# Optimization experiments

Measured on AMD Instinct MI355X. Metric: run time of the kernel, lower is better.

## Reference

```python
import jax, jax.numpy as jnp
import numpy as np

NEG_SLOPE = 0.2


def _gat_layer(x, src, dst, W, att_src, att_dst, bias, concat):
    # x: [N, Fin], W: [Fin, H*C], att_*: [H, C], bias: [H*C] or [C]
    N = x.shape[0]
    H, C = att_src.shape
    h = (x @ W).reshape(N, H, C)                      # node features per head
    a_src = jnp.sum(h * att_src, axis=-1)             # [N, H]
    a_dst = jnp.sum(h * att_dst, axis=-1)             # [N, H]
    e = jax.nn.leaky_relu(a_src[src] + a_dst[dst], NEG_SLOPE)  # [E, H]
    # segment softmax over destination nodes
    m = jax.ops.segment_max(e, dst, num_segments=N)   # [N, H]
    m = jnp.where(jnp.isfinite(m), m, 0.0)
    ex = jnp.exp(e - m[dst])
    s = jax.ops.segment_sum(ex, dst, num_segments=N)  # [N, H]
    alpha = ex / (s[dst] + 1e-16)                     # [E, H]
    msg = h[src] * alpha[:, :, None]                  # [E, H, C]
    out = jax.ops.segment_sum(msg, dst, num_segments=N)  # [N, H, C]
    out = out.reshape(N, H * C) if concat else out.mean(axis=1)
    return out + bias


def setup_inputs() -> dict:
    key = jax.random.key(0)
    ks = jax.random.split(key, 20)
    N, E, Fin, Cg, H = 50000, 800000, 128, 64, 4
    HC = H * Cg
    s = 0.1
    x = jax.random.normal(ks[0], (N, Fin), jnp.float32)
    edge_index = jax.random.randint(ks[1], (2, E), 0, N, dtype=jnp.int32)
    inp = {
        'x': x,
        'edge_index': edge_index,
        'W0': jax.random.normal(ks[2], (Fin, HC), jnp.float32) * s,
        'as0': jax.random.normal(ks[3], (H, Cg), jnp.float32) * s,
        'ad0': jax.random.normal(ks[4], (H, Cg), jnp.float32) * s,
        'b0': jnp.zeros((HC,), jnp.float32),
        'W1': jax.random.normal(ks[5], (HC, HC), jnp.float32) * s,
        'as1': jax.random.normal(ks[6], (H, Cg), jnp.float32) * s,
        'ad1': jax.random.normal(ks[7], (H, Cg), jnp.float32) * s,
        'b1': jnp.zeros((HC,), jnp.float32),
        'W2': jax.random.normal(ks[8], (HC, HC), jnp.float32) * s,
        'as2': jax.random.normal(ks[9], (H, Cg), jnp.float32) * s,
        'ad2': jax.random.normal(ks[10], (H, Cg), jnp.float32) * s,
        'b2': jnp.zeros((Cg,), jnp.float32),
        # linear head: 64 -> 128 -> 10
        'lw0': jax.random.normal(ks[11], (Cg, 128), jnp.float32) * s,
        'lb0': jnp.zeros((128,), jnp.float32),
        'lw1': jax.random.normal(ks[12], (128, 10), jnp.float32) * s,
        'lb1': jnp.zeros((10,), jnp.float32),
    }
    return inp


def reference(x, edge_index, W0, as0, ad0, b0, W1, as1, ad1, b1,
              W2, as2, ad2, b2, lw0, lb0, lw1, lb1):
    N = x.shape[0]
    # PyG GATConv add_self_loops=True: append self-loop edges
    loop = jnp.arange(N, dtype=edge_index.dtype)
    src = jnp.concatenate([edge_index[0], loop])
    dst = jnp.concatenate([edge_index[1], loop])
    h = _gat_layer(x, src, dst, W0, as0, ad0, b0, True)
    h = _gat_layer(h, src, dst, W1, as1, ad1, b1, True)
    h = _gat_layer(h, src, dst, W2, as2, ad2, b2, False)
    h = jax.nn.relu(h @ lw0 + lb0)
    return h @ lw1 + lb1
```

## Files before the change

kernel.cpp:

```cpp
#include <hip/hip_runtime.h>
#include <hip/hip_bf16.h>

#define HEADS 4
#define CH 64
#define HC 256

typedef __attribute__((ext_vector_type(8))) short short8;
typedef __attribute__((ext_vector_type(4))) float f32x4;
typedef __attribute__((ext_vector_type(8))) _Float16 half8;

__device__ inline unsigned short f2bf(float f){
  unsigned u = __float_as_uint(f);
  return (unsigned short)((u + 0x7FFF + ((u >> 16) & 1)) >> 16);
}


__global__ void hist_kernel(const int* __restrict__ dst, int E, int ET, int* __restrict__ cnt){
  int e = blockIdx.x * blockDim.x + threadIdx.x;
  if (e >= ET) return;
  int d = (e < E) ? dst[e] : (e - E);
  atomicAdd(&cnt[d], 1);
}

__global__ void blocksum_kernel(const int* __restrict__ cnt, int N, int* __restrict__ bsum){
  int tid = threadIdx.x;
  int i = blockIdx.x * 256 + tid;
  int v = (i < N) ? cnt[i] : 0;
  #pragma unroll
  for (int off = 32; off >= 1; off >>= 1) v += __shfl_xor(v, off);
  __shared__ int ws[4];
  if ((tid & 63) == 0) ws[tid >> 6] = v;
  __syncthreads();
  if (tid == 0) bsum[blockIdx.x] = ws[0] + ws[1] + ws[2] + ws[3];
}

__global__ void scanb_kernel(int* __restrict__ bsum, int nb){
  __shared__ int buf[256];
  int tid = threadIdx.x;
  int v = (tid < nb) ? bsum[tid] : 0;
  buf[tid] = v;
  __syncthreads();
  #pragma unroll
  for (int off = 1; off < 256; off <<= 1){
    int t = (tid >= off) ? buf[tid - off] : 0;
    __syncthreads();
    buf[tid] += t;
    __syncthreads();
  }
  if (tid < nb) bsum[tid] = buf[tid] - v;
}

__global__ void scanfinal_kernel(const int* __restrict__ cnt, const int* __restrict__ bsum,
                                 int* __restrict__ ptr, int* __restrict__ cur, int N){
  __shared__ int buf[256];
  int tid = threadIdx.x;
  int i = blockIdx.x * 256 + tid;
  int v = (i < N) ? cnt[i] : 0;
  buf[tid] = v;
  __syncthreads();
  #pragma unroll
  for (int off = 1; off < 256; off <<= 1){
    int t = (tid >= off) ? buf[tid - off] : 0;
    __syncthreads();
    buf[tid] += t;
    __syncthreads();
  }
  int exc = buf[tid] - v + bsum[blockIdx.x];
  if (i < N){
    ptr[i] = exc; cur[i] = exc;
    if (i == N - 1) ptr[N] = exc + v;
  }
}

__global__ void scatter_kernel(const int* __restrict__ src, const int* __restrict__ dst,
                               int E, int ET, int* __restrict__ cur, int* __restrict__ csr_src){
  int e = blockIdx.x * blockDim.x + threadIdx.x;
  if (e >= ET) return;
  int s, d;
  if (e < E){ s = src[e]; d = dst[e]; } else { s = e - E; d = e - E; }
  int pos = atomicAdd(&cur[d], 1);
  csr_src[pos] = s;
}


__global__ void wsplit_kernel(const float* __restrict__ W0, unsigned short* __restrict__ h0,
                              unsigned short* __restrict__ l0,
                              const float* __restrict__ W1, unsigned short* __restrict__ h1,
                              unsigned short* __restrict__ l1,
                              const float* __restrict__ W2, unsigned short* __restrict__ h2,
                              unsigned short* __restrict__ l2){
  int idx = blockIdx.x * 256 + threadIdx.x;
  const float* W; unsigned short *hi, *lo; int K;
  if (idx < 128 * HC){ W = W0; hi = h0; lo = l0; K = 128; }
  else if (idx < (128 + 256) * HC){ idx -= 128 * HC; W = W1; hi = h1; lo = l1; K = 256; }
  else { idx -= (128 + 256) * HC; W = W2; hi = h2; lo = l2; K = 256; }
  int k = idx >> 8, n = idx & 255;
  float w = W[idx];
  unsigned short hb = f2bf(w);
  float hf = __uint_as_float((unsigned)hb << 16);
  unsigned short lb = f2bf(w - hf);
  hi[(size_t)n * K + k] = hb;
  lo[(size_t)n * K + k] = lb;
}


__global__ void lwsplit_kernel(const float* __restrict__ lw0,
                               unsigned short* __restrict__ l0hi, unsigned short* __restrict__ l0lo,
                               const float* __restrict__ lw1, _Float16* __restrict__ l1T){
  int idx = blockIdx.x * 256 + threadIdx.x;
  if (idx < 8192){
    int n = idx & 127, k = idx >> 7;
    float w = lw0[k * 128 + n];
    unsigned short hb = f2bf(w);
    float hf = __uint_as_float((unsigned)hb << 16);
    unsigned short lb = f2bf(w - hf);
    l0hi[n * 64 + k] = hb;
    l0lo[n * 64 + k] = lb;
  } else if (idx < 8192 + 2048){
    int id = idx - 8192;
    int n = id & 15, k = id >> 4;
    float w = (n < 10) ? lw1[k * 10 + n] : 0.f;
    l1T[n * 128 + k] = (_Float16)w;
  }
}


__launch_bounds__(256, 2)
__global__ void gemm_mfma_kernel(const float* __restrict__ A,
                                 const unsigned short* __restrict__ BhiT,
                                 const unsigned short* __restrict__ BloT,
                                 _Float16* __restrict__ Cm,
                                 const float* __restrict__ att_s, const float* __restrict__ att_d,
                                 float* __restrict__ a_src, float* __restrict__ a_dst,
                                 int M, int K){
  __shared__ unsigned short As_hi[128][40];
  __shared__ unsigned short As_lo[128][40];
  __shared__ unsigned short Bs_hi[128][40];
  __shared__ unsigned short Bs_lo[128][40];

  int tid = threadIdx.x;
  int m0 = blockIdx.x * 128, n0 = blockIdx.y * 128;
  int wave = tid >> 6, lane = tid & 63;
  int wm = (wave >> 1) * 64, wn = (wave & 1) * 64;
  int col = lane & 15, quad = lane >> 4;

  f32x4 acc[4][4];
  #pragma unroll
  for (int a = 0; a < 4; a++)
    #pragma unroll
    for (int b = 0; b < 4; b++)
      acc[a][b] = (f32x4){0.f, 0.f, 0.f, 0.f};

  for (int k0 = 0; k0 < K; k0 += 32){
    #pragma unroll
    for (int r = 0; r < 2; r++){
      int id = r * 256 + tid;
      int m = id >> 2, q = id & 3;
      int gm = m0 + m;
      float va[8];
      if (gm < M){
        float4 v0 = *(const float4*)&A[(size_t)gm * K + k0 + q * 8];
        float4 v1 = *(const float4*)&A[(size_t)gm * K + k0 + q * 8 + 4];
        va[0]=v0.x; va[1]=v0.y; va[2]=v0.z; va[3]=v0.w;
        va[4]=v1.x; va[5]=v1.y; va[6]=v1.z; va[7]=v1.w;
      } else {
        #pragma unroll
        for (int j = 0; j < 8; j++) va[j] = 0.f;
      }
      short8 hi8, lo8;
      #pragma unroll
      for (int j = 0; j < 8; j++){
        unsigned short hb = f2bf(va[j]);
        float hf = __uint_as_float((unsigned)hb << 16);
        hi8[j] = (short)hb;
        lo8[j] = (short)f2bf(va[j] - hf);
      }
      *(short8*)&As_hi[m][q * 8] = hi8;
      *(short8*)&As_lo[m][q * 8] = lo8;
    }
    #pragma unroll
    for (int r = 0; r < 2; r++){
      int id = r * 256 + tid;
      int n = id >> 2, q = id & 3;
      size_t g = (size_t)(n0 + n) * K + k0 + q * 8;
      *(short8*)&Bs_hi[n][q * 8] = *(const short8*)&BhiT[g];
      *(short8*)&Bs_lo[n][q * 8] = *(const short8*)&BloT[g];
    }
    __syncthreads();

    short8 af[4][2], bf[4][2];
    #pragma unroll
    for (int t = 0; t < 4; t++){
      af[t][0] = *(const short8*)&As_hi[wm + t * 16 + col][quad * 8];
      af[t][1] = *(const short8*)&As_lo[wm + t * 16 + col][quad * 8];
      bf[t][0] = *(const short8*)&Bs_hi[wn + t * 16 + col][quad * 8];
      bf[t][1] = *(const short8*)&Bs_lo[wn + t * 16 + col][quad * 8];
    }
    #pragma unroll
    for (int mt = 0; mt < 4; mt++)
      #pragma unroll
      for (int nt = 0; nt < 4; nt++){
        acc[mt][nt] = __builtin_amdgcn_mfma_f32_16x16x32_bf16(af[mt][0], bf[nt][0], acc[mt][nt], 0, 0, 0);
        acc[mt][nt] = __builtin_amdgcn_mfma_f32_16x16x32_bf16(af[mt][1], bf[nt][0], acc[mt][nt], 0, 0, 0);
        acc[mt][nt] = __builtin_amdgcn_mfma_f32_16x16x32_bf16(af[mt][0], bf[nt][1], acc[mt][nt], 0, 0, 0);
      }
    __syncthreads();
  }

  #pragma unroll
  for (int mt = 0; mt < 4; mt++)
    #pragma unroll
    for (int nt = 0; nt < 4; nt++){
      int colg = n0 + wn + nt * 16 + col;
      #pragma unroll
      for (int r = 0; r < 4; r++){
        int row = m0 + wm + mt * 16 + quad * 4 + r;
        if (row < M) Cm[(size_t)row * HC + colg] = (_Float16)acc[mt][nt][r];
      }
    }

  int head = (n0 + wn) >> 6;
  float asv[4], adv[4];
  #pragma unroll
  for (int nt = 0; nt < 4; nt++){
    asv[nt] = att_s[head * CH + nt * 16 + col];
    adv[nt] = att_d[head * CH + nt * 16 + col];
  }
  #pragma unroll
  for (int mt = 0; mt < 4; mt++){
    float sp[4] = {0.f,0.f,0.f,0.f}, dp[4] = {0.f,0.f,0.f,0.f};
    #pragma unroll
    for (int nt = 0; nt < 4; nt++)
      #pragma unroll
      for (int r = 0; r < 4; r++){
        sp[r] += acc[mt][nt][r] * asv[nt];
        dp[r] += acc[mt][nt][r] * adv[nt];
      }
    #pragma unroll
    for (int off = 1; off <= 8; off <<= 1)
      #pragma unroll
      for (int r = 0; r < 4; r++){
        sp[r] += __shfl_xor(sp[r], off);
        dp[r] += __shfl_xor(dp[r], off);
      }
    if (col == 0){
      #pragma unroll
      for (int r = 0; r < 4; r++){
        int row = m0 + wm + mt * 16 + quad * 4 + r;
        if (row < M){
          a_src[row * HEADS + head] = sp[r];
          a_dst[row * HEADS + head] = dp[r];
        }
      }
    }
  }
}


__global__ void agg_kernel(const _Float16* __restrict__ h, const float* __restrict__ a_src,
                           const float* __restrict__ a_dst, const int* __restrict__ ptr,
                           const int* __restrict__ csr_src, const float* __restrict__ bias,
                           float* __restrict__ out, int N, int mean_mode,
                           const float* __restrict__ b2){
  __shared__ float sm[HEADS][CH];
  int n = blockIdx.x;
  int head = threadIdx.x >> 6;
  int lane = threadIdx.x & 63;
  int eg = lane >> 3, c8 = lane & 7;
  int beg = ptr[n], end = ptr[n + 1];
  float adst = a_dst[n * HEADS + head];

  float acc[8] = {0.f,0.f,0.f,0.f,0.f,0.f,0.f,0.f};
  float ss = 0.f;
  for (int i = beg + eg; i < end; i += 8){
    int s = csr_src[i];
    float e = a_src[s * HEADS + head] + adst;
    e = e > 0.f ? e : 0.2f * e;
    float w = __expf(e);
    half8 hv = *(const half8*)&h[(size_t)s * HC + head * CH + c8 * 8];
    #pragma unroll
    for (int j = 0; j < 8; j++) acc[j] += w * (float)hv[j];
    ss += w;
  }
  #pragma unroll
  for (int off = 8; off <= 32; off <<= 1){
    #pragma unroll
    for (int j = 0; j < 8; j++) acc[j] += __shfl_xor(acc[j], off);
    ss += __shfl_xor(ss, off);
  }
  float inv = 1.f / (ss + 1e-16f);
  #pragma unroll
  for (int j = 0; j < 8; j++) acc[j] *= inv;

  if (!mean_mode){
    if (eg == 0){
      float* op = &out[(size_t)n * HC + head * CH + c8 * 8];
      const float* bp = &bias[head * CH + c8 * 8];
      #pragma unroll
      for (int j = 0; j < 8; j++) op[j] = acc[j] + bp[j];
    }
  } else {
    if (eg == 0){
      #pragma unroll
      for (int j = 0; j < 8; j++) sm[head][c8 * 8 + j] = acc[j];
    }
    __syncthreads();
    int t = threadIdx.x;
    if (t < CH)
      out[(size_t)n * CH + t] =
        0.25f * (sm[0][t] + sm[1][t] + sm[2][t] + sm[3][t]) + b2[t];
  }
}


__launch_bounds__(256, 2)
__global__ void head_mfma_kernel(const float* __restrict__ f2,
                                 const unsigned short* __restrict__ lw0hiT,
                                 const unsigned short* __restrict__ lw0loT,
                                 const _Float16* __restrict__ lw1T,
                                 const float* __restrict__ lb0,
                                 const float* __restrict__ lb1,
                                 float* __restrict__ outp, int N){
  __shared__ __align__(16) unsigned short L[27648];
  __shared__ __align__(16) _Float16 Ls[16][136];
  const int tid = threadIdx.x;
  const int wave = tid >> 6, lane = tid & 63;
  const int col = lane & 15, quad = lane >> 4;
  const int m0 = blockIdx.x * 64;

  { int n = tid >> 4, k = (tid & 15) * 8;
    *(half8*)&Ls[n][k] = *(const half8*)&lw1T[n * 128 + k]; }

  #pragma unroll
  for (int r = 0; r < 2; r++){
    int id = r * 256 + tid;
    int m = id >> 3, q = id & 7;
    int gm = m0 + m;
    float va[8];
    if (gm < N){
      float4 v0 = *(const float4*)&f2[(size_t)gm * CH + q * 8];
      float4 v1 = *(const float4*)&f2[(size_t)gm * CH + q * 8 + 4];
      va[0]=v0.x; va[1]=v0.y; va[2]=v0.z; va[3]=v0.w;
      va[4]=v1.x; va[5]=v1.y; va[6]=v1.z; va[7]=v1.w;
    } else {
      #pragma unroll
      for (int j = 0; j < 8; j++) va[j] = 0.f;
    }
    short8 hi8, lo8;
    #pragma unroll
    for (int j = 0; j < 8; j++){
      unsigned short hb = f2bf(va[j]);
      float hf = __uint_as_float((unsigned)hb << 16);
      hi8[j] = (short)hb;
      lo8[j] = (short)f2bf(va[j] - hf);
    }
    *(short8*)&L[m * 72 + q * 8] = hi8;
    *(short8*)&L[4608 + m * 72 + q * 8] = lo8;
  }
  #pragma unroll
  for (int r = 0; r < 4; r++){
    int id = r * 256 + tid;
    int n = id >> 3, q = id & 7;
    *(short8*)&L[9216 + n * 72 + q * 8]  = *(const short8*)&lw0hiT[n * 64 + q * 8];
    *(short8*)&L[18432 + n * 72 + q * 8] = *(const short8*)&lw0loT[n * 64 + q * 8];
  }
  __syncthreads();

  const int wn = wave * 32;
  f32x4 acc[4][2];
  #pragma unroll
  for (int a = 0; a < 4; a++)
    #pragma unroll
    for (int b = 0; b < 2; b++) acc[a][b] = (f32x4){0.f,0.f,0.f,0.f};

  #pragma unroll
  for (int ks = 0; ks < 2; ks++){
    int k = ks * 32 + quad * 8;
    short8 ah[4], al[4], bh[2], bl[2];
    #pragma unroll
    for (int mt = 0; mt < 4; mt++){
      ah[mt] = *(short8*)&L[(mt * 16 + col) * 72 + k];
      al[mt] = *(short8*)&L[4608 + (mt * 16 + col) * 72 + k];
    }
    #pragma unroll
    for (int nt = 0; nt < 2; nt++){
      bh[nt] = *(short8*)&L[9216 + (wn + nt * 16 + col) * 72 + k];
      bl[nt] = *(short8*)&L[18432 + (wn + nt * 16 + col) * 72 + k];
    }
    #pragma unroll
    for (int mt = 0; mt < 4; mt++)
      #pragma unroll
      for (int nt = 0; nt < 2; nt++){
        acc[mt][nt] = __builtin_amdgcn_mfma_f32_16x16x32_bf16(ah[mt], bh[nt], acc[mt][nt], 0, 0, 0);
        acc[mt][nt] = __builtin_amdgcn_mfma_f32_16x16x32_bf16(al[mt], bh[nt], acc[mt][nt], 0, 0, 0);
        acc[mt][nt] = __builtin_amdgcn_mfma_f32_16x16x32_bf16(ah[mt], bl[nt], acc[mt][nt], 0, 0, 0);
      }
  }
  __syncthreads();

  _Float16* Zp = (_Float16*)L;
  #pragma unroll
  for (int nt = 0; nt < 2; nt++){
    int n = wn + nt * 16 + col;
    float b = lb0[n];
    #pragma unroll
    for (int mt = 0; mt < 4; mt++)
      #pragma unroll
      for (int r2 = 0; r2 < 4; r2++){
        int m = mt * 16 + quad * 4 + r2;
        float z = acc[mt][nt][r2] + b;
        Zp[m * 136 + n] = (_Float16)fmaxf(z, 0.f);
      }
  }
  __syncthreads();

  f32x4 acc2 = (f32x4){0.f,0.f,0.f,0.f};
  #pragma unroll
  for (int ks = 0; ks < 4; ks++){
    int k = ks * 32 + quad * 8;
    half8 a2 = *(half8*)&Zp[(wave * 16 + col) * 136 + k];
    half8 b2v = *(half8*)&Ls[col][k];
    acc2 = __builtin_amdgcn_mfma_f32_16x16x32_f16(a2, b2v, acc2, 0, 0, 0);
  }
  if (col < 10){
    float bb = lb1[col];
    #pragma unroll
    for (int r2 = 0; r2 < 4; r2++){
      int row = m0 + wave * 16 + quad * 4 + r2;
      if (row < N) outp[(size_t)row * 10 + col] = acc2[r2] + bb;
    }
  }
}


extern "C" void kernel_launch(void* const* d_in, const int* in_sizes, int n_in,
                              void* d_out, int out_size, void* d_ws, size_t ws_size,
                              hipStream_t stream) {
  const float* x   = (const float*)d_in[0];
  const int*   ei  = (const int*)d_in[1];
  const float* W0  = (const float*)d_in[2];
  const float* as0 = (const float*)d_in[3];
  const float* ad0 = (const float*)d_in[4];
  const float* b0  = (const float*)d_in[5];
  const float* W1  = (const float*)d_in[6];
  const float* as1 = (const float*)d_in[7];
  const float* ad1 = (const float*)d_in[8];
  const float* b1  = (const float*)d_in[9];
  const float* W2  = (const float*)d_in[10];
  const float* as2 = (const float*)d_in[11];
  const float* ad2 = (const float*)d_in[12];
  const float* b2  = (const float*)d_in[13];
  const float* lw0 = (const float*)d_in[14];
  const float* lb0 = (const float*)d_in[15];
  const float* lw1 = (const float*)d_in[16];
  const float* lb1 = (const float*)d_in[17];
  float* outp = (float*)d_out;

  int N  = in_sizes[0] / 128;
  int E  = in_sizes[1] / 2;
  int ET = E + N;
  int nb = (N + 255) / 256;

  char* ws = (char*)d_ws;
  float* F       = (float*)ws;    ws += (size_t)N * HC * sizeof(float);
  _Float16* Hb   = (_Float16*)ws; ws += (size_t)N * HC * sizeof(_Float16);
  float* a_s = (float*)ws; ws += (size_t)N * HEADS * sizeof(float);
  float* a_d = (float*)ws; ws += (size_t)N * HEADS * sizeof(float);
  int* cnt   = (int*)ws;   ws += (size_t)N * sizeof(int);
  int* cur   = (int*)ws;   ws += (size_t)N * sizeof(int);
  int* ptrA  = (int*)ws;   ws += (size_t)(N + 1) * sizeof(int);
  int* bsum  = (int*)ws;   ws += (size_t)nb * sizeof(int);
  int* csr   = (int*)ws;   ws += (size_t)ET * sizeof(int);
  unsigned short* w0hi = (unsigned short*)ws; ws += (size_t)128 * HC * 2;
  unsigned short* w0lo = (unsigned short*)ws; ws += (size_t)128 * HC * 2;
  unsigned short* w1hi = (unsigned short*)ws; ws += (size_t)HC * HC * 2;
  unsigned short* w1lo = (unsigned short*)ws; ws += (size_t)HC * HC * 2;
  unsigned short* w2hi = (unsigned short*)ws; ws += (size_t)HC * HC * 2;
  unsigned short* w2lo = (unsigned short*)ws; ws += (size_t)HC * HC * 2;
  unsigned short* l0hi = (unsigned short*)ws; ws += (size_t)8192 * 2;
  unsigned short* l0lo = (unsigned short*)ws; ws += (size_t)8192 * 2;
  _Float16* l1T        = (_Float16*)ws;       ws += (size_t)2048 * 2;
  float* f2  = F;

  const int* srcArr = ei;
  const int* dstArr = ei + E;

  hipMemsetAsync(cnt, 0, (size_t)N * sizeof(int), stream);
  hist_kernel<<<(ET + 255) / 256, 256, 0, stream>>>(dstArr, E, ET, cnt);
  blocksum_kernel<<<nb, 256, 0, stream>>>(cnt, N, bsum);
  scanb_kernel<<<1, 256, 0, stream>>>(bsum, nb);
  scanfinal_kernel<<<nb, 256, 0, stream>>>(cnt, bsum, ptrA, cur, N);
  scatter_kernel<<<(ET + 255) / 256, 256, 0, stream>>>(srcArr, dstArr, E, ET, cur, csr);

  wsplit_kernel<<<((128 + 256 + 256) * HC) / 256, 256, 0, stream>>>(
      W0, w0hi, w0lo, W1, w1hi, w1lo, W2, w2hi, w2lo);
  lwsplit_kernel<<<(8192 + 2048 + 255) / 256, 256, 0, stream>>>(lw0, l0hi, l0lo, lw1, l1T);

  dim3 ggrid((N + 127) / 128, 2);

  gemm_mfma_kernel<<<ggrid, 256, 0, stream>>>(x, w0hi, w0lo, Hb, as0, ad0, a_s, a_d, N, 128);
  agg_kernel<<<N, 256, 0, stream>>>(Hb, a_s, a_d, ptrA, csr, b0, F, N, 0, nullptr);

  gemm_mfma_kernel<<<ggrid, 256, 0, stream>>>(F, w1hi, w1lo, Hb, as1, ad1, a_s, a_d, N, HC);
  agg_kernel<<<N, 256, 0, stream>>>(Hb, a_s, a_d, ptrA, csr, b1, F, N, 0, nullptr);

  gemm_mfma_kernel<<<ggrid, 256, 0, stream>>>(F, w2hi, w2lo, Hb, as2, ad2, a_s, a_d, N, HC);
  agg_kernel<<<N, 256, 0, stream>>>(Hb, a_s, a_d, ptrA, csr, nullptr, f2, N, 1, b2);

  head_mfma_kernel<<<(N + 63) / 64, 256, 0, stream>>>(f2, l0hi, l0lo, l1T, lb0, lb1, outp, N);
}
```

Before: 595.8 us.

## Pre-split GEMM inputs into bf16 hi/lo in producers and unroll aggregation loop

The bf16 hi/lo split of the GEMM A operand moves out of the GEMM load path. The aggregation kernel now writes hi/lo bf16 pairs directly, and a new xsplit kernel pre-splits x for the first layer. The GEMM then loads short8 halves straight into shared memory, so each of the two column blocks no longer repeats the conversion arithmetic. Separately, the aggregation edge loop is unrolled by two with independent accumulators to expose more memory-level parallelism. The cost is an extra pass over x for the split kernel, plus a separate f2 buffer for the last layer's output.

```diff
diff --git a/kernel.cpp b/kernel.cpp
--- a/kernel.cpp
+++ b/kernel.cpp
@@ -104,6 +104,25 @@
 }
 
 
+__global__ void xsplit_kernel(const float* __restrict__ x, int total4,
+                              unsigned short* __restrict__ xhi, unsigned short* __restrict__ xlo){
+  int i4 = blockIdx.x * 256 + threadIdx.x;
+  if (i4 >= total4) return;
+  float4 v = *(const float4*)&x[(size_t)i4 * 4];
+  float va[4] = {v.x, v.y, v.z, v.w};
+  unsigned short h4[4], l4[4];
+  #pragma unroll
+  for (int j = 0; j < 4; j++){
+    unsigned short hb = f2bf(va[j]);
+    float hf = __uint_as_float((unsigned)hb << 16);
+    h4[j] = hb;
+    l4[j] = f2bf(va[j] - hf);
+  }
+  *(ushort4*)&xhi[(size_t)i4 * 4] = make_ushort4(h4[0], h4[1], h4[2], h4[3]);
+  *(ushort4*)&xlo[(size_t)i4 * 4] = make_ushort4(l4[0], l4[1], l4[2], l4[3]);
+}
+
+
 __global__ void lwsplit_kernel(const float* __restrict__ lw0,
                                unsigned short* __restrict__ l0hi, unsigned short* __restrict__ l0lo,
                                const float* __restrict__ lw1, _Float16* __restrict__ l1T){
@@ -126,7 +145,8 @@
 
 
 __launch_bounds__(256, 2)
-__global__ void gemm_mfma_kernel(const float* __restrict__ A,
+__global__ void gemm_mfma_kernel(const unsigned short* __restrict__ Ahi,
+                                 const unsigned short* __restrict__ Alo,
                                  const unsigned short* __restrict__ BhiT,
                                  const unsigned short* __restrict__ BloT,
                                  _Float16* __restrict__ Cm,
@@ -151,32 +171,22 @@
     for (int b = 0; b < 4; b++)
       acc[a][b] = (f32x4){0.f, 0.f, 0.f, 0.f};
 
+  const short8 zero8 = (short8){0,0,0,0,0,0,0,0};
+
   for (int k0 = 0; k0 < K; k0 += 32){
     #pragma unroll
     for (int r = 0; r < 2; r++){
       int id = r * 256 + tid;
       int m = id >> 2, q = id & 3;
       int gm = m0 + m;
-      float va[8];
+      size_t g = (size_t)gm * K + k0 + q * 8;
+      short8 vh = zero8, vl = zero8;
       if (gm < M){
-        float4 v0 = *(const float4*)&A[(size_t)gm * K + k0 + q * 8];
-        float4 v1 = *(const float4*)&A[(size_t)gm * K + k0 + q * 8 + 4];
-        va[0]=v0.x; va[1]=v0.y; va[2]=v0.z; va[3]=v0.w;
-        va[4]=v1.x; va[5]=v1.y; va[6]=v1.z; va[7]=v1.w;
-      } else {
-        #pragma unroll
-        for (int j = 0; j < 8; j++) va[j] = 0.f;
-      }
-      short8 hi8, lo8;
-      #pragma unroll
-      for (int j = 0; j < 8; j++){
-        unsigned short hb = f2bf(va[j]);
-        float hf = __uint_as_float((unsigned)hb << 16);
-        hi8[j] = (short)hb;
-        lo8[j] = (short)f2bf(va[j] - hf);
-      }
-      *(short8*)&As_hi[m][q * 8] = hi8;
-      *(short8*)&As_lo[m][q * 8] = lo8;
+        vh = *(const short8*)&Ahi[g];
+        vl = *(const short8*)&Alo[g];
+      }
+      *(short8*)&As_hi[m][q * 8] = vh;
+      *(short8*)&As_lo[m][q * 8] = vl;
     }
     #pragma unroll
     for (int r = 0; r < 2; r++){
@@ -260,8 +270,9 @@
 __global__ void agg_kernel(const _Float16* __restrict__ h, const float* __restrict__ a_src,
                            const float* __restrict__ a_dst, const int* __restrict__ ptr,
                            const int* __restrict__ csr_src, const float* __restrict__ bias,
-                           float* __restrict__ out, int N, int mean_mode,
-                           const float* __restrict__ b2){
+                           unsigned short* __restrict__ out_hi, unsigned short* __restrict__ out_lo,
+                           int N, int mean_mode, const float* __restrict__ b2,
+                           float* __restrict__ f2){
   __shared__ float sm[HEADS][CH];
   int n = blockIdx.x;
   int head = threadIdx.x >> 6;
@@ -270,18 +281,40 @@
   int beg = ptr[n], end = ptr[n + 1];
   float adst = a_dst[n * HEADS + head];
 
-  float acc[8] = {0.f,0.f,0.f,0.f,0.f,0.f,0.f,0.f};
-  float ss = 0.f;
-  for (int i = beg + eg; i < end; i += 8){
-    int s = csr_src[i];
-    float e = a_src[s * HEADS + head] + adst;
-    e = e > 0.f ? e : 0.2f * e;
-    float w = __expf(e);
-    half8 hv = *(const half8*)&h[(size_t)s * HC + head * CH + c8 * 8];
-    #pragma unroll
-    for (int j = 0; j < 8; j++) acc[j] += w * (float)hv[j];
-    ss += w;
-  }
+  float acc0[8] = {0.f,0.f,0.f,0.f,0.f,0.f,0.f,0.f};
+  float acc1[8] = {0.f,0.f,0.f,0.f,0.f,0.f,0.f,0.f};
+  float ss0 = 0.f, ss1 = 0.f;
+  int i = beg + eg;
+  for (; i + 8 < end; i += 16){
+    int s0 = csr_src[i], s1 = csr_src[i + 8];
+    float e0 = a_src[s0 * HEADS + head] + adst;
+    float e1 = a_src[s1 * HEADS + head] + adst;
+    e0 = e0 > 0.f ? e0 : 0.2f * e0;
+    e1 = e1 > 0.f ? e1 : 0.2f * e1;
+    float w0 = __expf(e0), w1 = __expf(e1);
+    half8 h0 = *(const half8*)&h[(size_t)s0 * HC + head * CH + c8 * 8];
+    half8 h1 = *(const half8*)&h[(size_t)s1 * HC + head * CH + c8 * 8];
+    #pragma unroll
+    for (int j = 0; j < 8; j++){
+      acc0[j] += w0 * (float)h0[j];
+      acc1[j] += w1 * (float)h1[j];
+    }
+    ss0 += w0; ss1 += w1;
+  }
+  if (i < end){
+    int s0 = csr_src[i];
+    float e0 = a_src[s0 * HEADS + head] + adst;
+    e0 = e0 > 0.f ? e0 : 0.2f * e0;
+    float w0 = __expf(e0);
+    half8 h0 = *(const half8*)&h[(size_t)s0 * HC + head * CH + c8 * 8];
+    #pragma unroll
+    for (int j = 0; j < 8; j++) acc0[j] += w0 * (float)h0[j];
+    ss0 += w0;
+  }
+  float ss = ss0 + ss1;
+  float acc[8];
+  #pragma unroll
+  for (int j = 0; j < 8; j++) acc[j] = acc0[j] + acc1[j];
   #pragma unroll
   for (int off = 8; off <= 32; off <<= 1){
     #pragma unroll
@@ -294,10 +327,19 @@
 
   if (!mean_mode){
     if (eg == 0){
-      float* op = &out[(size_t)n * HC + head * CH + c8 * 8];
       const float* bp = &bias[head * CH + c8 * 8];
-      #pragma unroll
-      for (int j = 0; j < 8; j++) op[j] = acc[j] + bp[j];
+      short8 hi8, lo8;
+      #pragma unroll
+      for (int j = 0; j < 8; j++){
+        float v = acc[j] + bp[j];
+        unsigned short hb = f2bf(v);
+        float hf = __uint_as_float((unsigned)hb << 16);
+        hi8[j] = (short)hb;
+        lo8[j] = (short)f2bf(v - hf);
+      }
+      size_t o = (size_t)n * HC + head * CH + c8 * 8;
+      *(short8*)&out_hi[o] = hi8;
+      *(short8*)&out_lo[o] = lo8;
     }
   } else {
     if (eg == 0){
@@ -307,7 +349,7 @@
     __syncthreads();
     int t = threadIdx.x;
     if (t < CH)
-      out[(size_t)n * CH + t] =
+      f2[(size_t)n * CH + t] =
         0.25f * (sm[0][t] + sm[1][t] + sm[2][t] + sm[3][t]) + b2[t];
   }
 }
@@ -462,8 +504,10 @@
   int nb = (N + 255) / 256;
 
   char* ws = (char*)d_ws;
-  float* F       = (float*)ws;    ws += (size_t)N * HC * sizeof(float);
-  _Float16* Hb   = (_Float16*)ws; ws += (size_t)N * HC * sizeof(_Float16);
+  _Float16* Hb = (_Float16*)ws;       ws += (size_t)N * HC * sizeof(_Float16);
+  unsigned short* Fhi = (unsigned short*)ws; ws += (size_t)N * HC * 2;
+  unsigned short* Flo = (unsigned short*)ws; ws += (size_t)N * HC * 2;
+  float* f2  = (float*)ws; ws += (size_t)N * CH * sizeof(float);
   float* a_s = (float*)ws; ws += (size_t)N * HEADS * sizeof(float);
   float* a_d = (float*)ws; ws += (size_t)N * HEADS * sizeof(float);
   int* cnt   = (int*)ws;   ws += (size_t)N * sizeof(int);
@@ -480,7 +524,6 @@
   unsigned short* l0hi = (unsigned short*)ws; ws += (size_t)8192 * 2;
   unsigned short* l0lo = (unsigned short*)ws; ws += (size_t)8192 * 2;
   _Float16* l1T        = (_Float16*)ws;       ws += (size_t)2048 * 2;
-  float* f2  = F;
 
   const int* srcArr = ei;
   const int* dstArr = ei + E;
@@ -495,17 +538,18 @@
   wsplit_kernel<<<((128 + 256 + 256) * HC) / 256, 256, 0, stream>>>(
       W0, w0hi, w0lo, W1, w1hi, w1lo, W2, w2hi, w2lo);
   lwsplit_kernel<<<(8192 + 2048 + 255) / 256, 256, 0, stream>>>(lw0, l0hi, l0lo, lw1, l1T);
+  xsplit_kernel<<<(N * 128 / 4 + 255) / 256, 256, 0, stream>>>(x, N * 128 / 4, Fhi, Flo);
 
   dim3 ggrid((N + 127) / 128, 2);
 
-  gemm_mfma_kernel<<<ggrid, 256, 0, stream>>>(x, w0hi, w0lo, Hb, as0, ad0, a_s, a_d, N, 128);
-  agg_kernel<<<N, 256, 0, stream>>>(Hb, a_s, a_d, ptrA, csr, b0, F, N, 0, nullptr);
-
-  gemm_mfma_kernel<<<ggrid, 256, 0, stream>>>(F, w1hi, w1lo, Hb, as1, ad1, a_s, a_d, N, HC);
-  agg_kernel<<<N, 256, 0, stream>>>(Hb, a_s, a_d, ptrA, csr, b1, F, N, 0, nullptr);
-
-  gemm_mfma_kernel<<<ggrid, 256, 0, stream>>>(F, w2hi, w2lo, Hb, as2, ad2, a_s, a_d, N, HC);
-  agg_kernel<<<N, 256, 0, stream>>>(Hb, a_s, a_d, ptrA, csr, nullptr, f2, N, 1, b2);
+  gemm_mfma_kernel<<<ggrid, 256, 0, stream>>>(Fhi, Flo, w0hi, w0lo, Hb, as0, ad0, a_s, a_d, N, 128);
+  agg_kernel<<<N, 256, 0, stream>>>(Hb, a_s, a_d, ptrA, csr, b0, Fhi, Flo, N, 0, nullptr, nullptr);
+
+  gemm_mfma_kernel<<<ggrid, 256, 0, stream>>>(Fhi, Flo, w1hi, w1lo, Hb, as1, ad1, a_s, a_d, N, HC);
+  agg_kernel<<<N, 256, 0, stream>>>(Hb, a_s, a_d, ptrA, csr, b1, Fhi, Flo, N, 0, nullptr, nullptr);
+
+  gemm_mfma_kernel<<<ggrid, 256, 0, stream>>>(Fhi, Flo, w2hi, w2lo, Hb, as2, ad2, a_s, a_d, N, HC);
+  agg_kernel<<<N, 256, 0, stream>>>(Hb, a_s, a_d, ptrA, csr, nullptr, nullptr, nullptr, N, 1, b2, f2);
 
   head_mfma_kernel<<<(N + 63) / 64, 256, 0, stream>>>(f2, l0hi, l0lo, l1T, lb0, lb1, outp, N);
 }
```

New measurement: 593.8 us. Within noise of the previous version (-0.3%).
